# Optimization experiments

Hardware: AMD Instinct MI355X
Metric: run time of the kernel (lower is better)

Reference implementation:

```python
import jax, jax.numpy as jnp
import numpy as np

N = 50000        # nodes
E = 800000       # edges (before self-loops)
F_IN = 128       # input features
HID = 32         # per-head hidden channels
H1 = 4           # heads of conv1
H2 = 8           # heads of conv2
NEG_SLOPE = 0.2  # PyG GATConv LeakyReLU slope
E_DEC = 100000   # pos/neg decode edges each


def setup_inputs() -> dict:
    key = jax.random.key(0)
    ks = jax.random.split(key, 12)
    s = 0.1
    return {
        "x": jax.random.normal(ks[0], (N, F_IN), jnp.float32),
        "edge_index": jax.random.randint(ks[1], (2, E), 0, N, dtype=jnp.int32),
        "pos_edge_index": jax.random.randint(ks[2], (2, E_DEC), 0, N, dtype=jnp.int32),
        "neg_edge_index": jax.random.randint(ks[3], (2, E_DEC), 0, N, dtype=jnp.int32),
        "W1": jax.random.normal(ks[4], (F_IN, H1 * HID), jnp.float32) * s,
        "a_src1": jax.random.normal(ks[5], (H1, HID), jnp.float32) * s,
        "a_dst1": jax.random.normal(ks[6], (H1, HID), jnp.float32) * s,
        "b1": jax.random.normal(ks[7], (H1 * HID,), jnp.float32) * s,
        "W2": jax.random.normal(ks[8], (H1 * HID, H2 * HID), jnp.float32) * s,
        "a_src2": jax.random.normal(ks[9], (H2, HID), jnp.float32) * s,
        "a_dst2": jax.random.normal(ks[10], (H2, HID), jnp.float32) * s,
        "b2": jax.random.normal(ks[11], (H2 * HID,), jnp.float32) * s,
    }


def _segment_softmax(e, seg, n):
    # softmax over edges grouped by destination node; max is detached (cancels analytically)
    m = jax.lax.stop_gradient(jax.ops.segment_max(e, seg, num_segments=n))
    ex = jnp.exp(e - m[seg])
    denom = jax.ops.segment_sum(ex, seg, num_segments=n)
    return ex / (denom[seg] + 1e-16)


def _gat_conv(x, src, dst, W, a_src, a_dst, b, heads, out_ch):
    n = x.shape[0]
    h = (x @ W).reshape(n, heads, out_ch)             # [N,H,C]
    al_s = (h * a_src[None]).sum(-1)                  # [N,H]
    al_d = (h * a_dst[None]).sum(-1)                  # [N,H]
    e = al_s[src] + al_d[dst]                         # [E,H] edge logits
    e = jnp.where(e > 0, e, NEG_SLOPE * e)            # LeakyReLU
    alpha = _segment_softmax(e, dst, n)               # [E,H]
    msg = h[src] * alpha[:, :, None]                  # [E,H,C]
    out = jax.ops.segment_sum(msg, dst, num_segments=n)  # [N,H,C]
    return out.reshape(n, heads * out_ch) + b


def reference(x, edge_index, pos_edge_index, neg_edge_index,
              W1, a_src1, a_dst1, b1, W2, a_src2, a_dst2, b2):
    n = x.shape[0]
    loops = jnp.arange(n, dtype=edge_index.dtype)     # PyG add_self_loops=True
    src = jnp.concatenate([edge_index[0], loops])
    dst = jnp.concatenate([edge_index[1], loops])
    # encode
    z = jax.nn.relu(_gat_conv(x, src, dst, W1, a_src1, a_dst1, b1, H1, HID))
    z = _gat_conv(z, src, dst, W2, a_src2, a_dst2, b2, H2, HID)
    # decode
    ei = jnp.concatenate([pos_edge_index, neg_edge_index], axis=1)
    logits = (z[ei[0]] * z[ei[1]]).sum(-1)            # [2*E_DEC]
    return logits
```

## Files before the change

kernel.cpp:

```cpp
#include <hip/hip_runtime.h>
#include <hip/hip_bf16.h>

#define NN 50000
#define EE 800000
#define ET (EE + NN)
#define F_IN 128
#define HID 32
#define H1 4
#define H2 8
#define E_DEC 100000
#define NEG_SLOPE 0.2f

typedef __attribute__((ext_vector_type(8))) short short8;
typedef __attribute__((ext_vector_type(4))) float floatx4;

__device__ __forceinline__ unsigned short f2b(float f) {
    __hip_bfloat16 h = __float2bfloat16(f);
    return *reinterpret_cast<unsigned short*>(&h);
}
__device__ __forceinline__ float b2f(unsigned short u) {
    return __uint_as_float(((unsigned int)u) << 16);
}

__device__ __forceinline__ void packW_one(const float* __restrict__ W,
                                          unsigned short* __restrict__ Wp, int OUT, int id) {
    const int ctg = id >> 8;
    const int ln = id & 63;
    const int col = ctg * 16 + (ln & 15);
    const int k0 = ((id >> 6) & 3) * 32 + ((ln >> 4) & 3) * 8;
    ushort4 lo, hi;
    lo.x = f2b(W[(k0 + 0) * OUT + col]);
    lo.y = f2b(W[(k0 + 1) * OUT + col]);
    lo.z = f2b(W[(k0 + 2) * OUT + col]);
    lo.w = f2b(W[(k0 + 3) * OUT + col]);
    hi.x = f2b(W[(k0 + 4) * OUT + col]);
    hi.y = f2b(W[(k0 + 5) * OUT + col]);
    hi.z = f2b(W[(k0 + 6) * OUT + col]);
    hi.w = f2b(W[(k0 + 7) * OUT + col]);
    ((ushort4*)Wp)[id * 2] = lo;
    ((ushort4*)Wp)[id * 2 + 1] = hi;
}

#define HIST_BLOCKS ((EE / 4 + 255) / 256)
#define PACK_BLOCKS ((6144 + 255) / 256)

__global__ void hist_pack_k(const int* __restrict__ ei, int* __restrict__ counts,
                            const float* __restrict__ W1, unsigned short* __restrict__ wp1,
                            const float* __restrict__ W2, unsigned short* __restrict__ wp2) {
    if (blockIdx.x < HIST_BLOCKS) {
        const int t = blockIdx.x * 256 + threadIdx.x;
        if (t >= EE / 4) return;
        const int4 d4 = ((const int4*)(ei + EE))[t];
        atomicAdd(&counts[d4.x], 1);
        atomicAdd(&counts[d4.y], 1);
        atomicAdd(&counts[d4.z], 1);
        atomicAdd(&counts[d4.w], 1);
    } else {
        const int id = (blockIdx.x - HIST_BLOCKS) * 256 + threadIdx.x;
        if (id < 2048) packW_one(W1, wp1, 128, id);
        else if (id < 6144) packW_one(W2, wp2, 256, id - 2048);
    }
}

__global__ void scan1_k(const int* __restrict__ counts, const int* __restrict__ probe,
                        int* __restrict__ bsum) {
    __shared__ int sh[256];
    const int pv = probe[0];
    int t = threadIdx.x;
    int i = blockIdx.x * 256 + t;
    sh[t] = (i < NN) ? (counts[i] - pv + 1) : 0;
    __syncthreads();
    for (int off = 128; off > 0; off >>= 1) {
        if (t < off) sh[t] += sh[t + off];
        __syncthreads();
    }
    if (t == 0) bsum[blockIdx.x] = sh[0];
}

__global__ void scan2_k(int* __restrict__ bsum, int nb, int* __restrict__ start) {
    __shared__ int sh[256];
    int t = threadIdx.x;
    int v = (t < nb) ? bsum[t] : 0;
    sh[t] = v;
    __syncthreads();
    for (int off = 1; off < 256; off <<= 1) {
        int u = (t >= off) ? sh[t - off] : 0;
        __syncthreads();
        sh[t] += u;
        __syncthreads();
    }
    if (t < nb) bsum[t] = sh[t] - v;
    if (t == 0) start[NN] = ET;
}

__global__ void scan3_k(const int* __restrict__ counts, const int* __restrict__ probe,
                        const int* __restrict__ bsum, int* __restrict__ start,
                        int* __restrict__ cursor) {
    __shared__ int sh[256];
    const int pv = probe[0];
    int t = threadIdx.x;
    int i = blockIdx.x * 256 + t;
    int c = (i < NN) ? (counts[i] - pv + 1) : 0;
    sh[t] = c;
    __syncthreads();
    for (int off = 1; off < 256; off <<= 1) {
        int u = (t >= off) ? sh[t - off] : 0;
        __syncthreads();
        sh[t] += u;
        __syncthreads();
    }
    int excl = sh[t] - c + bsum[blockIdx.x];
    if (i < NN) {
        start[i] = excl;
        cursor[i] = excl;
    }
}

__global__ void scatter_k(const int* __restrict__ ei, int* __restrict__ cursor,
                          int* __restrict__ csr) {
    const int NT_E = EE / 4;
    const int t = blockIdx.x * blockDim.x + threadIdx.x;
    if (t < NT_E) {
        const int4 s4 = ((const int4*)ei)[t];
        const int4 d4 = ((const int4*)(ei + EE))[t];
        csr[atomicAdd(&cursor[d4.x], 1)] = s4.x;
        csr[atomicAdd(&cursor[d4.y], 1)] = s4.y;
        csr[atomicAdd(&cursor[d4.z], 1)] = s4.z;
        csr[atomicAdd(&cursor[d4.w], 1)] = s4.w;
    } else {
        const int j = (t - NT_E) * 4;
#pragma unroll
        for (int k = 0; k < 4; ++k) {
            const int n = j + k;
            if (n < NN) csr[atomicAdd(&cursor[n], 1)] = n;
        }
    }
}

template <int OUT, int H, int CT, bool F32IN, int HSCH>
__global__ void gemm_k(const void* __restrict__ Xin, const unsigned short* __restrict__ Wp,
                       const float* __restrict__ a_src, const float* __restrict__ a_dst,
                       unsigned short* __restrict__ Hout, float* __restrict__ als,
                       float* __restrict__ ald) {
    const int wave = threadIdx.x >> 6;
    const int lane = threadIdx.x & 63;
    const int quad = lane >> 4;
    const int rl = lane & 15;
    const int r0 = blockIdx.x * 64;
    floatx4 acc[4][CT];
#pragma unroll
    for (int rt = 0; rt < 4; ++rt)
#pragma unroll
        for (int ct = 0; ct < CT; ++ct) acc[rt][ct] = {0.f, 0.f, 0.f, 0.f};

#pragma unroll
    for (int ks = 0; ks < 4; ++ks) {
        short8 a[4];
        const int c0k = ks * 32 + quad * 8;
#pragma unroll
        for (int rt = 0; rt < 4; ++rt) {
            int row = r0 + rt * 16 + rl;
            row = row < NN ? row : NN - 1;
            if (F32IN) {
                const float4* xp =
                    (const float4*)((const float*)Xin + (long long)row * 128 + c0k);
                const float4 v0 = xp[0];
                const float4 v1 = xp[1];
                short8 tt;
                tt[0] = (short)f2b(v0.x);
                tt[1] = (short)f2b(v0.y);
                tt[2] = (short)f2b(v0.z);
                tt[3] = (short)f2b(v0.w);
                tt[4] = (short)f2b(v1.x);
                tt[5] = (short)f2b(v1.y);
                tt[6] = (short)f2b(v1.z);
                tt[7] = (short)f2b(v1.w);
                a[rt] = tt;
            } else {
                a[rt] = *(const short8*)((const unsigned short*)Xin +
                                         (long long)row * 128 + c0k);
            }
        }
#pragma unroll
        for (int ct = 0; ct < CT; ++ct) {
            const int ctg = wave * CT + ct;
            const short8 b = *(const short8*)(Wp + (((ctg * 4 + ks) * 64 + lane) << 3));
#pragma unroll
            for (int rt = 0; rt < 4; ++rt)
                acc[rt][ct] = __builtin_amdgcn_mfma_f32_16x16x32_bf16(a[rt], b, acc[rt][ct], 0, 0, 0);
        }
    }
#pragma unroll
    for (int rt = 0; rt < 4; ++rt) {
        const int rowbase = r0 + rt * 16 + quad * 4;
#pragma unroll
        for (int ct = 0; ct < CT; ++ct) {
            const int col = (wave * CT + ct) * 16 + rl;
            const long long sb = (long long)(col / HSCH) * NN * HSCH + (col % HSCH);
#pragma unroll
            for (int r = 0; r < 4; ++r) {
                const int row = rowbase + r;
                if (row < NN) Hout[sb + (long long)row * HSCH] = f2b(acc[rt][ct][r]);
            }
        }
    }
    float asv[CT], adv[CT];
#pragma unroll
    for (int ct = 0; ct < CT; ++ct) {
        const int col = (wave * CT + ct) * 16 + rl;
        asv[ct] = a_src[col];
        adv[ct] = a_dst[col];
    }
#pragma unroll
    for (int rt = 0; rt < 4; ++rt) {
#pragma unroll
        for (int r = 0; r < 4; ++r) {
            const int row = r0 + rt * 16 + quad * 4 + r;
            float ps[CT / 2], pd[CT / 2];
#pragma unroll
            for (int hh = 0; hh < CT / 2; ++hh) {
                ps[hh] = acc[rt][2 * hh][r] * asv[2 * hh] + acc[rt][2 * hh + 1][r] * asv[2 * hh + 1];
                pd[hh] = acc[rt][2 * hh][r] * adv[2 * hh] + acc[rt][2 * hh + 1][r] * adv[2 * hh + 1];
#pragma unroll
                for (int m = 8; m >= 1; m >>= 1) {
                    ps[hh] += __shfl_xor(ps[hh], m, 64);
                    pd[hh] += __shfl_xor(pd[hh], m, 64);
                }
            }
            if (rl == 0 && row < NN) {
#pragma unroll
                for (int hh = 0; hh < CT / 2; ++hh) {
                    const int hd = wave * (CT / 2) + hh;
                    als[(long long)hd * NN + row] = ps[hh];
                    ald[(long long)hd * NN + row] = pd[hh];
                }
            }
        }
    }
}

__global__ void gather1_k(const int* __restrict__ start, const int* __restrict__ csr,
                          const float* __restrict__ als, const float* __restrict__ ald,
                          const unsigned short* __restrict__ Hin,
                          const float* __restrict__ bias, unsigned short* __restrict__ outp) {
    const int d = blockIdx.x;
    const int lane = threadIdx.x;
    const int cl = lane & 31;
    const int slot = lane >> 5;
    const int hd = cl >> 3;
    const float* alsh = als + (long long)hd * NN;
    const int beg = start[d], end = start[d + 1];
    const float aldd = ald[(long long)hd * NN + d];
    float a0 = 0.f, a1 = 0.f, a2 = 0.f, a3 = 0.f, den = 0.f;
    int i = beg + slot;
    for (; i + 7 * 2 < end; i += 8 * 2) {
        int s[8];
        float l[8];
        ushort4 hv[8];
#pragma unroll
        for (int k = 0; k < 8; ++k) s[k] = csr[i + k * 2];
#pragma unroll
        for (int k = 0; k < 8; ++k) l[k] = alsh[s[k]] + aldd;
#pragma unroll
        for (int k = 0; k < 8; ++k) hv[k] = *(const ushort4*)(Hin + (long long)s[k] * 128 + cl * 4);
#pragma unroll
        for (int k = 0; k < 8; ++k) {
            float lg = l[k] > 0.f ? l[k] : NEG_SLOPE * l[k];
            const float w = __expf(lg);
            den += w;
            a0 += w * b2f(hv[k].x);
            a1 += w * b2f(hv[k].y);
            a2 += w * b2f(hv[k].z);
            a3 += w * b2f(hv[k].w);
        }
    }
    for (; i + 3 * 2 < end; i += 4 * 2) {
        int s[4];
        float l[4];
        ushort4 hv[4];
#pragma unroll
        for (int k = 0; k < 4; ++k) s[k] = csr[i + k * 2];
#pragma unroll
        for (int k = 0; k < 4; ++k) l[k] = alsh[s[k]] + aldd;
#pragma unroll
        for (int k = 0; k < 4; ++k) hv[k] = *(const ushort4*)(Hin + (long long)s[k] * 128 + cl * 4);
#pragma unroll
        for (int k = 0; k < 4; ++k) {
            float lg = l[k] > 0.f ? l[k] : NEG_SLOPE * l[k];
            const float w = __expf(lg);
            den += w;
            a0 += w * b2f(hv[k].x);
            a1 += w * b2f(hv[k].y);
            a2 += w * b2f(hv[k].z);
            a3 += w * b2f(hv[k].w);
        }
    }
    for (; i < end; i += 2) {
        const int s = csr[i];
        float lg = alsh[s] + aldd;
        lg = lg > 0.f ? lg : NEG_SLOPE * lg;
        const float w = __expf(lg);
        const ushort4 hv = *(const ushort4*)(Hin + (long long)s * 128 + cl * 4);
        den += w;
        a0 += w * b2f(hv.x);
        a1 += w * b2f(hv.y);
        a2 += w * b2f(hv.z);
        a3 += w * b2f(hv.w);
    }
    a0 += __shfl_xor(a0, 32, 64);
    a1 += __shfl_xor(a1, 32, 64);
    a2 += __shfl_xor(a2, 32, 64);
    a3 += __shfl_xor(a3, 32, 64);
    den += __shfl_xor(den, 32, 64);
    if (lane < 32) {
        const float inv = 1.f / (den + 1e-16f);
        const int c0 = cl * 4;
        float v0 = a0 * inv + bias[c0];
        float v1 = a1 * inv + bias[c0 + 1];
        float v2 = a2 * inv + bias[c0 + 2];
        float v3 = a3 * inv + bias[c0 + 3];
        v0 = v0 > 0.f ? v0 : 0.f;
        v1 = v1 > 0.f ? v1 : 0.f;
        v2 = v2 > 0.f ? v2 : 0.f;
        v3 = v3 > 0.f ? v3 : 0.f;
        ushort4 o;
        o.x = f2b(v0);
        o.y = f2b(v1);
        o.z = f2b(v2);
        o.w = f2b(v3);
        *(ushort4*)(outp + (long long)d * 128 + c0) = o;
    }
}

__global__ void gather2s_k(const int* __restrict__ start, const int* __restrict__ csr,
                           const float* __restrict__ als, const float* __restrict__ ald,
                           const unsigned short* __restrict__ h2s,
                           const float* __restrict__ bias, unsigned short* __restrict__ z2) {
    const int s = blockIdx.x & 7;
    const int g = blockIdx.x >> 3;
    const int wave = threadIdx.x >> 6;
    const int lane = threadIdx.x & 63;
    const int slot = lane >> 3;
    const int cl = lane & 7;
    const int d = g * 32 + wave * 8 + slot;
    if (d >= NN) return;
    const float* alsh = als + (long long)s * NN;
    const unsigned short* hsl = h2s + (long long)s * NN * 32 + cl * 4;
    const int beg = start[d], end = start[d + 1];
    const float aldd = ald[(long long)s * NN + d];
    float a0 = 0.f, a1 = 0.f, a2 = 0.f, a3 = 0.f, den = 0.f;
    int i = beg;
    for (; i + 3 < end; i += 4) {
        int sx[4];
        float l[4];
        ushort4 hv[4];
#pragma unroll
        for (int k = 0; k < 4; ++k) sx[k] = csr[i + k];
#pragma unroll
        for (int k = 0; k < 4; ++k) l[k] = alsh[sx[k]] + aldd;
#pragma unroll
        for (int k = 0; k < 4; ++k) hv[k] = *(const ushort4*)(hsl + (long long)sx[k] * 32);
#pragma unroll
        for (int k = 0; k < 4; ++k) {
            float lg = l[k] > 0.f ? l[k] : NEG_SLOPE * l[k];
            const float w = __expf(lg);
            den += w;
            a0 += w * b2f(hv[k].x);
            a1 += w * b2f(hv[k].y);
            a2 += w * b2f(hv[k].z);
            a3 += w * b2f(hv[k].w);
        }
    }
    for (; i < end; ++i) {
        const int sx = csr[i];
        float lg = alsh[sx] + aldd;
        lg = lg > 0.f ? lg : NEG_SLOPE * lg;
        const float w = __expf(lg);
        const ushort4 hv = *(const ushort4*)(hsl + (long long)sx * 32);
        den += w;
        a0 += w * b2f(hv.x);
        a1 += w * b2f(hv.y);
        a2 += w * b2f(hv.z);
        a3 += w * b2f(hv.w);
    }
    const float inv = 1.f / (den + 1e-16f);
    const float4 bv = *(const float4*)(bias + s * 32 + cl * 4);
    ushort4 o;
    o.x = f2b(a0 * inv + bv.x);
    o.y = f2b(a1 * inv + bv.y);
    o.z = f2b(a2 * inv + bv.z);
    o.w = f2b(a3 * inv + bv.w);
    *(ushort4*)(z2 + (long long)d * 256 + s * 32 + cl * 4) = o;
}

__global__ void decode_k(const int* __restrict__ pei, const int* __restrict__ nei,
                         const unsigned short* __restrict__ z2, float* __restrict__ out) {
    const int wave = threadIdx.x >> 6, lane = threadIdx.x & 63;
    const int base = blockIdx.x * 8 + wave * 2;
    int av[2], bv[2];
    bool ok[2];
#pragma unroll
    for (int k = 0; k < 2; ++k) {
        const int idx = base + k;
        ok[k] = idx < 2 * E_DEC;
        int a = 0, b = 0;
        if (ok[k]) {
            if (idx < E_DEC) {
                a = pei[idx];
                b = pei[E_DEC + idx];
            } else {
                const int j = idx - E_DEC;
                a = nei[j];
                b = nei[E_DEC + j];
            }
        }
        av[k] = a;
        bv[k] = b;
    }
    ushort4 ua[2], ub[2];
#pragma unroll
    for (int k = 0; k < 2; ++k) {
        ua[k] = *(const ushort4*)(z2 + (long long)av[k] * 256 + lane * 4);
        ub[k] = *(const ushort4*)(z2 + (long long)bv[k] * 256 + lane * 4);
    }
#pragma unroll
    for (int k = 0; k < 2; ++k) {
        float s = b2f(ua[k].x) * b2f(ub[k].x) + b2f(ua[k].y) * b2f(ub[k].y) +
                  b2f(ua[k].z) * b2f(ub[k].z) + b2f(ua[k].w) * b2f(ub[k].w);
#pragma unroll
        for (int m = 32; m >= 1; m >>= 1) s += __shfl_xor(s, m, 64);
        if (lane == 0 && ok[k]) out[base + k] = s;
    }
}

extern "C" void kernel_launch(void* const* d_in, const int* in_sizes, int n_in,
                              void* d_out, int out_size, void* d_ws, size_t ws_size,
                              hipStream_t stream) {
    const float* x = (const float*)d_in[0];
    const int* ei = (const int*)d_in[1];
    const int* pei = (const int*)d_in[2];
    const int* nei = (const int*)d_in[3];
    const float* W1 = (const float*)d_in[4];
    const float* as1 = (const float*)d_in[5];
    const float* ad1 = (const float*)d_in[6];
    const float* b1 = (const float*)d_in[7];
    const float* W2 = (const float*)d_in[8];
    const float* as2 = (const float*)d_in[9];
    const float* ad2 = (const float*)d_in[10];
    const float* b2 = (const float*)d_in[11];
    float* out = (float*)d_out;

    unsigned short* h1 = (unsigned short*)d_ws;
    unsigned short* h2s = h1 + (long long)NN * 128;
    unsigned short* z2 = h2s + (long long)NN * 256;
    unsigned short* z1 = z2 + (long long)NN * 256;
    unsigned short* wp1 = z1 + (long long)NN * 128;
    unsigned short* wp2 = wp1 + 128 * 128;
    float* als1 = (float*)(wp2 + 128 * 256);
    float* ald1 = als1 + NN * H1;
    float* als2 = ald1 + NN * H1;
    float* ald2 = als2 + NN * H2;
    int* counts = (int*)(ald2 + NN * H2);
    int* start = counts + NN;
    int* cursor = start + NN + 1;
    int* bsum = cursor + NN;
    int* csr = bsum + 256;
    int* probe = csr + ET;

    const int NB = (NN + 255) / 256;

    hist_pack_k<<<HIST_BLOCKS + PACK_BLOCKS, 256, 0, stream>>>(ei, counts, W1, wp1, W2, wp2);
    scan1_k<<<NB, 256, 0, stream>>>(counts, probe, bsum);
    scan2_k<<<1, 256, 0, stream>>>(bsum, NB, start);
    scan3_k<<<NB, 256, 0, stream>>>(counts, probe, bsum, start, cursor);
    {
        const int nt = EE / 4 + (NN + 3) / 4;
        scatter_k<<<(nt + 255) / 256, 256, 0, stream>>>(ei, cursor, csr);
    }

    gemm_k<128, H1, 2, true, 128><<<(NN + 63) / 64, 256, 0, stream>>>(
        x, wp1, as1, ad1, h1, als1, ald1);
    gather1_k<<<NN, 64, 0, stream>>>(start, csr, als1, ald1, h1, b1, z1);

    gemm_k<256, H2, 4, false, 32><<<(NN + 63) / 64, 256, 0, stream>>>(
        z1, wp2, as2, ad2, h2s, als2, ald2);
    gather2s_k<<<8 * ((NN + 31) / 32), 256, 0, stream>>>(
        start, csr, als2, ald2, h2s, b2, z2);

    decode_k<<<(2 * E_DEC + 7) / 8, 256, 0, stream>>>(pei, nei, z2, out);
}
```

Before: 374.1 us.

## Move head slicing from layer-2 gather to decode with partial-sum reduction

The layer-2 projection output goes back to row-major [N,256], and layer-2 aggregation now uses one 64-lane block per destination node with an 8-wide unrolled edge loop. Head-sliced processing moves to the decode stage instead: each 32-column slice computes partial dot products into a workspace buffer, and a new reduce kernel sums the 8 partials. This trades the per-slice L2 locality of the gather for slice locality in decode, which gathers random rows of z2. The cost is an extra partial buffer and one more kernel launch.

After: 377.0 us. About the same (+0.8%).

```diff
diff --git a/kernel.cpp b/kernel.cpp
--- a/kernel.cpp
+++ b/kernel.cpp
@@ -137,7 +137,7 @@
     }
 }
 
-template <int OUT, int H, int CT, bool F32IN, int HSCH>
+template <int OUT, int H, int CT, bool F32IN>
 __global__ void gemm_k(const void* __restrict__ Xin, const unsigned short* __restrict__ Wp,
                        const float* __restrict__ a_src, const float* __restrict__ a_dst,
                        unsigned short* __restrict__ Hout, float* __restrict__ als,
@@ -196,11 +196,10 @@
 #pragma unroll
         for (int ct = 0; ct < CT; ++ct) {
             const int col = (wave * CT + ct) * 16 + rl;
-            const long long sb = (long long)(col / HSCH) * NN * HSCH + (col % HSCH);
 #pragma unroll
             for (int r = 0; r < 4; ++r) {
                 const int row = rowbase + r;
-                if (row < NN) Hout[sb + (long long)row * HSCH] = f2b(acc[rt][ct][r]);
+                if (row < NN) Hout[(long long)row * OUT + col] = f2b(acc[rt][ct][r]);
             }
         }
     }
@@ -332,34 +331,49 @@
     }
 }
 
-__global__ void gather2s_k(const int* __restrict__ start, const int* __restrict__ csr,
-                           const float* __restrict__ als, const float* __restrict__ ald,
-                           const unsigned short* __restrict__ h2s,
-                           const float* __restrict__ bias, unsigned short* __restrict__ z2) {
-    const int s = blockIdx.x & 7;
-    const int g = blockIdx.x >> 3;
-    const int wave = threadIdx.x >> 6;
-    const int lane = threadIdx.x & 63;
-    const int slot = lane >> 3;
-    const int cl = lane & 7;
-    const int d = g * 32 + wave * 8 + slot;
-    if (d >= NN) return;
-    const float* alsh = als + (long long)s * NN;
-    const unsigned short* hsl = h2s + (long long)s * NN * 32 + cl * 4;
+__global__ void gather2_k(const int* __restrict__ start, const int* __restrict__ csr,
+                          const float* __restrict__ als, const float* __restrict__ ald,
+                          const unsigned short* __restrict__ Hin,
+                          const float* __restrict__ bias, unsigned short* __restrict__ outp) {
+    const int d = blockIdx.x;
+    const int lane = threadIdx.x;
+    const int hd = lane >> 3;
+    const float* alsh = als + (long long)hd * NN;
     const int beg = start[d], end = start[d + 1];
-    const float aldd = ald[(long long)s * NN + d];
+    const float aldd = ald[(long long)hd * NN + d];
     float a0 = 0.f, a1 = 0.f, a2 = 0.f, a3 = 0.f, den = 0.f;
     int i = beg;
+    for (; i + 7 < end; i += 8) {
+        int s[8];
+        float l[8];
+        ushort4 hv[8];
+#pragma unroll
+        for (int k = 0; k < 8; ++k) s[k] = csr[i + k];
+#pragma unroll
+        for (int k = 0; k < 8; ++k) l[k] = alsh[s[k]] + aldd;
+#pragma unroll
+        for (int k = 0; k < 8; ++k) hv[k] = *(const ushort4*)(Hin + (long long)s[k] * 256 + lane * 4);
+#pragma unroll
+        for (int k = 0; k < 8; ++k) {
+            float lg = l[k] > 0.f ? l[k] : NEG_SLOPE * l[k];
+            const float w = __expf(lg);
+            den += w;
+            a0 += w * b2f(hv[k].x);
+            a1 += w * b2f(hv[k].y);
+            a2 += w * b2f(hv[k].z);
+            a3 += w * b2f(hv[k].w);
+        }
+    }
     for (; i + 3 < end; i += 4) {
-        int sx[4];
+        int s[4];
         float l[4];
         ushort4 hv[4];
 #pragma unroll
-        for (int k = 0; k < 4; ++k) sx[k] = csr[i + k];
-#pragma unroll
-        for (int k = 0; k < 4; ++k) l[k] = alsh[sx[k]] + aldd;
-#pragma unroll
-        for (int k = 0; k < 4; ++k) hv[k] = *(const ushort4*)(hsl + (long long)sx[k] * 32);
+        for (int k = 0; k < 4; ++k) s[k] = csr[i + k];
+#pragma unroll
+        for (int k = 0; k < 4; ++k) l[k] = alsh[s[k]] + aldd;
+#pragma unroll
+        for (int k = 0; k < 4; ++k) hv[k] = *(const ushort4*)(Hin + (long long)s[k] * 256 + lane * 4);
 #pragma unroll
         for (int k = 0; k < 4; ++k) {
             float lg = l[k] > 0.f ? l[k] : NEG_SLOPE * l[k];
@@ -372,11 +386,11 @@
         }
     }
     for (; i < end; ++i) {
-        const int sx = csr[i];
-        float lg = alsh[sx] + aldd;
+        const int s = csr[i];
+        float lg = alsh[s] + aldd;
         lg = lg > 0.f ? lg : NEG_SLOPE * lg;
         const float w = __expf(lg);
-        const ushort4 hv = *(const ushort4*)(hsl + (long long)sx * 32);
+        const ushort4 hv = *(const ushort4*)(Hin + (long long)s * 256 + lane * 4);
         den += w;
         a0 += w * b2f(hv.x);
         a1 += w * b2f(hv.y);
@@ -384,53 +398,49 @@
         a3 += w * b2f(hv.w);
     }
     const float inv = 1.f / (den + 1e-16f);
-    const float4 bv = *(const float4*)(bias + s * 32 + cl * 4);
+    const int c0 = lane * 4;
     ushort4 o;
-    o.x = f2b(a0 * inv + bv.x);
-    o.y = f2b(a1 * inv + bv.y);
-    o.z = f2b(a2 * inv + bv.z);
-    o.w = f2b(a3 * inv + bv.w);
-    *(ushort4*)(z2 + (long long)d * 256 + s * 32 + cl * 4) = o;
-}
-
-__global__ void decode_k(const int* __restrict__ pei, const int* __restrict__ nei,
-                         const unsigned short* __restrict__ z2, float* __restrict__ out) {
+    o.x = f2b(a0 * inv + bias[c0]);
+    o.y = f2b(a1 * inv + bias[c0 + 1]);
+    o.z = f2b(a2 * inv + bias[c0 + 2]);
+    o.w = f2b(a3 * inv + bias[c0 + 3]);
+    *(ushort4*)(outp + (long long)d * 256 + c0) = o;
+}
+
+__global__ void decode_s_k(const int* __restrict__ pei, const int* __restrict__ nei,
+                           const unsigned short* __restrict__ z2, float* __restrict__ part) {
+    const int s = blockIdx.x & 7;
+    const int g = blockIdx.x >> 3;
     const int wave = threadIdx.x >> 6, lane = threadIdx.x & 63;
-    const int base = blockIdx.x * 8 + wave * 2;
-    int av[2], bv[2];
-    bool ok[2];
-#pragma unroll
-    for (int k = 0; k < 2; ++k) {
-        const int idx = base + k;
-        ok[k] = idx < 2 * E_DEC;
-        int a = 0, b = 0;
-        if (ok[k]) {
-            if (idx < E_DEC) {
-                a = pei[idx];
-                b = pei[E_DEC + idx];
-            } else {
-                const int j = idx - E_DEC;
-                a = nei[j];
-                b = nei[E_DEC + j];
-            }
-        }
-        av[k] = a;
-        bv[k] = b;
-    }
-    ushort4 ua[2], ub[2];
-#pragma unroll
-    for (int k = 0; k < 2; ++k) {
-        ua[k] = *(const ushort4*)(z2 + (long long)av[k] * 256 + lane * 4);
-        ub[k] = *(const ushort4*)(z2 + (long long)bv[k] * 256 + lane * 4);
-    }
-#pragma unroll
-    for (int k = 0; k < 2; ++k) {
-        float s = b2f(ua[k].x) * b2f(ub[k].x) + b2f(ua[k].y) * b2f(ub[k].y) +
-                  b2f(ua[k].z) * b2f(ub[k].z) + b2f(ua[k].w) * b2f(ub[k].w);
-#pragma unroll
-        for (int m = 32; m >= 1; m >>= 1) s += __shfl_xor(s, m, 64);
-        if (lane == 0 && ok[k]) out[base + k] = s;
-    }
+    const int slot = lane >> 3, cl = lane & 7;
+    const int idx = g * 32 + wave * 8 + slot;
+    if (idx >= 2 * E_DEC) return;
+    int a, b;
+    if (idx < E_DEC) {
+        a = pei[idx];
+        b = pei[E_DEC + idx];
+    } else {
+        const int j = idx - E_DEC;
+        a = nei[j];
+        b = nei[E_DEC + j];
+    }
+    const ushort4 ua = *(const ushort4*)(z2 + (long long)a * 256 + s * 32 + cl * 4);
+    const ushort4 ub = *(const ushort4*)(z2 + (long long)b * 256 + s * 32 + cl * 4);
+    float sum = b2f(ua.x) * b2f(ub.x) + b2f(ua.y) * b2f(ub.y) +
+                b2f(ua.z) * b2f(ub.z) + b2f(ua.w) * b2f(ub.w);
+    sum += __shfl_xor(sum, 4, 64);
+    sum += __shfl_xor(sum, 2, 64);
+    sum += __shfl_xor(sum, 1, 64);
+    if (cl == 0) part[(long long)s * (2 * E_DEC) + idx] = sum;
+}
+
+__global__ void reduce_k(const float* __restrict__ part, float* __restrict__ out) {
+    const int i = blockIdx.x * 256 + threadIdx.x;
+    if (i >= 2 * E_DEC) return;
+    float s = 0.f;
+#pragma unroll
+    for (int k = 0; k < 8; ++k) s += part[(long long)k * (2 * E_DEC) + i];
+    out[i] = s;
 }
 
 extern "C" void kernel_launch(void* const* d_in, const int* in_sizes, int n_in,
@@ -451,8 +461,8 @@
     float* out = (float*)d_out;
 
     unsigned short* h1 = (unsigned short*)d_ws;
-    unsigned short* h2s = h1 + (long long)NN * 128;
-    unsigned short* z2 = h2s + (long long)NN * 256;
+    unsigned short* h2 = h1 + (long long)NN * 128;
+    unsigned short* z2 = h2 + (long long)NN * 256;
     unsigned short* z1 = z2 + (long long)NN * 256;
     unsigned short* wp1 = z1 + (long long)NN * 128;
     unsigned short* wp2 = wp1 + 128 * 128;
@@ -460,7 +470,8 @@
     float* ald1 = als1 + NN * H1;
     float* als2 = ald1 + NN * H1;
     float* ald2 = als2 + NN * H2;
-    int* counts = (int*)(ald2 + NN * H2);
+    float* part = ald2 + NN * H2;
+    int* counts = (int*)(part + 8 * 2 * E_DEC);
     int* start = counts + NN;
     int* cursor = start + NN + 1;
     int* bsum = cursor + NN;
@@ -478,14 +489,14 @@
         scatter_k<<<(nt + 255) / 256, 256, 0, stream>>>(ei, cursor, csr);
     }
 
-    gemm_k<128, H1, 2, true, 128><<<(NN + 63) / 64, 256, 0, stream>>>(
+    gemm_k<128, H1, 2, true><<<(NN + 63) / 64, 256, 0, stream>>>(
         x, wp1, as1, ad1, h1, als1, ald1);
     gather1_k<<<NN, 64, 0, stream>>>(start, csr, als1, ald1, h1, b1, z1);
 
-    gemm_k<256, H2, 4, false, 32><<<(NN + 63) / 64, 256, 0, stream>>>(
-        z1, wp2, as2, ad2, h2s, als2, ald2);
-    gather2s_k<<<8 * ((NN + 31) / 32), 256, 0, stream>>>(
-        start, csr, als2, ald2, h2s, b2, z2);
-
-    decode_k<<<(2 * E_DEC + 7) / 8, 256, 0, stream>>>(pei, nei, z2, out);
-}
+    gemm_k<256, H2, 4, false><<<(NN + 63) / 64, 256, 0, stream>>>(
+        z1, wp2, as2, ad2, h2, als2, ald2);
+    gather2_k<<<NN, 64, 0, stream>>>(start, csr, als2, ald2, h2, b2, z2);
+
+    decode_s_k<<<8 * ((2 * E_DEC + 31) / 32), 256, 0, stream>>>(pei, nei, z2, part);
+    reduce_k<<<(2 * E_DEC + 255) / 256, 256, 0, stream>>>(part, out);
+}
```
